# Performance work log

Measured on AMD Instinct MI355X. Metric: run time of the kernel, lower is better.

Reference implementation:

```python
import jax, jax.numpy as jnp
import numpy as np
import math

B, T, D = 8, 1024, 512
WS = 12          # window_size (top-k)
EPS = 1e-5       # BatchNorm eps (eval mode, running stats)
NEG = -1e9


def setup_inputs() -> dict:
    key = jax.random.key(0)
    ks = jax.random.split(key, 13)
    x = jax.random.normal(ks[0], (B, T, D), jnp.float32)
    conv1_w = jax.random.normal(ks[1], (512, 512, 5, 5), jnp.float32) / np.float32(np.sqrt(512 * 25))
    conv1_b = jax.random.normal(ks[2], (512,), jnp.float32) * 0.01
    bn1_g = jax.random.uniform(ks[3], (512,), jnp.float32, 0.5, 1.5)
    bn1_b = jax.random.normal(ks[4], (512,), jnp.float32) * 0.1
    bn1_m = jax.random.normal(ks[5], (512,), jnp.float32) * 0.1
    bn1_v = jax.random.uniform(ks[6], (512,), jnp.float32, 0.5, 1.5)
    conv2_w = jax.random.normal(ks[7], (512, 512, 5, 3), jnp.float32) / np.float32(np.sqrt(512 * 15))
    conv2_b = jax.random.normal(ks[8], (512,), jnp.float32) * 0.01
    bn2_g = jax.random.uniform(ks[9], (512,), jnp.float32, 0.5, 1.5)
    bn2_b = jax.random.normal(ks[10], (512,), jnp.float32) * 0.1
    bn2_m = jax.random.normal(ks[11], (512,), jnp.float32) * 0.1
    bn2_v = jax.random.uniform(ks[12], (512,), jnp.float32, 0.5, 1.5)
    return dict(x=x, conv1_w=conv1_w, conv1_b=conv1_b, bn1_g=bn1_g, bn1_b=bn1_b,
                bn1_m=bn1_m, bn1_v=bn1_v, conv2_w=conv2_w, conv2_b=conv2_b,
                bn2_g=bn2_g, bn2_b=bn2_b, bn2_m=bn2_m, bn2_v=bn2_v)


def _conv_nchw(h, w, b):
    # Conv2d padding=(2,0): pad height by 2 each side, no width padding.
    out = jax.lax.conv_general_dilated(h, w, window_strides=(1, 1),
                                       padding=((2, 2), (0, 0)),
                                       dimension_numbers=('NCHW', 'OIHW', 'NCHW'))
    return out + b[None, :, None, None]


def _bn(h, g, bt, m, v):
    # eval-mode BatchNorm2d with running stats
    inv = jax.lax.rsqrt(v + EPS)
    return (h - m[None, :, None, None]) * (g * inv)[None, :, None, None] + bt[None, :, None, None]


def _pool2(h):
    return jax.lax.reduce_window(h, -jnp.inf, jax.lax.max,
                                 (1, 1, 2, 2), (1, 1, 2, 2), 'VALID')


def reference(x, conv1_w, conv1_b, bn1_g, bn1_b, bn1_m, bn1_v,
              conv2_w, conv2_b, bn2_g, bn2_b, bn2_m, bn2_v):
    b, t, d = x.shape
    # masked local attention scores
    scores = jnp.einsum('btd,bsd->bts', x, x) / math.sqrt(d)  # [B,T,T]
    i = jnp.arange(t)[:, None]
    j = jnp.arange(t)[None, :]
    band = jnp.abs(j - i) <= (WS - 1)  # local band, width 2*WS-1
    scores = jnp.where(band[None], scores, NEG)
    # top-k window select, indices sorted ascending
    _, idx = jax.lax.top_k(scores, WS)           # [B,T,WS]
    ids = jnp.sort(idx, axis=-1)
    # batched gather: out[b,t,k,:] = x[b, ids[b,t,k], :]
    gathered = x[jnp.arange(b)[:, None, None], ids]  # [B,T,WS,D]
    h = gathered.transpose(0, 3, 1, 2)               # [B,512,T,WS]
    # conv encoder
    h = jax.nn.relu(_bn(_conv_nchw(h, conv1_w, conv1_b), bn1_g, bn1_b, bn1_m, bn1_v))
    h = _pool2(h)                                    # [B,512,T/2,4]
    h = jax.nn.relu(_bn(_conv_nchw(h, conv2_w, conv2_b), bn2_g, bn2_b, bn2_m, bn2_v))
    h = _pool2(h)                                    # [B,512,T/4,1]
    return jnp.squeeze(h)                            # [B,512,T/4]
```

## Files before the change

### kernel.cpp

```cpp
#include <hip/hip_runtime.h>
#include <hip/hip_bf16.h>

typedef short bf16x8 __attribute__((ext_vector_type(8)));
typedef float f32x16 __attribute__((ext_vector_type(16)));
typedef unsigned short u16;

__device__ __forceinline__ u16 f2bf(float v) {
    union { __hip_bfloat16 h; u16 u; } cv;
    cv.h = __float2bfloat16(v);
    return cv.u;
}

__device__ __forceinline__ void gld_lds16(const u16* g, u16* l) {
    __builtin_amdgcn_global_load_lds(
        (const __attribute__((address_space(1))) void*)g,
        (__attribute__((address_space(3))) void*)l, 16, 0, 0);
}

__global__ void prep_w1(const float* __restrict__ w, u16* __restrict__ o) {
    int idx = blockIdx.x * 256 + threadIdx.x;
    if (idx >= 25 * 512 * 512) return;
    int e = idx & 7, ocl = (idx >> 3) & 63, c = (idx >> 9) & 3;
    int ocs = (idx >> 11) & 7, T = idx >> 14;
    int icb = T / 25, tap = T - icb * 25;
    int ic = icb * 32 + c * 8 + e;
    int oc = ocs * 64 + ocl;
    int kh = tap / 5, kw = tap - kh * 5;
    o[idx] = f2bf(w[(((size_t)oc * 512 + ic) * 5 + kh) * 5 + kw]);
}

__global__ void prep_w2(const float* __restrict__ w, u16* __restrict__ o) {
    int idx = blockIdx.x * 256 + threadIdx.x;
    if (idx >= 15 * 512 * 512) return;
    int e = idx & 7, ocl = (idx >> 3) & 63, c = (idx >> 9) & 3;
    int ocs = (idx >> 11) & 7, T = idx >> 14;
    int icb = T / 15, tap = T - icb * 15;
    int ic = icb * 32 + c * 8 + e;
    int oc = ocs * 64 + ocl;
    int kh = tap / 3, kw = tap - kh * 3;
    o[idx] = f2bf(w[(((size_t)oc * 512 + ic) * 5 + kh) * 3 + kw]);
}

__global__ void prep_bn(const float* __restrict__ g, const float* __restrict__ b,
                        const float* __restrict__ m, const float* __restrict__ v,
                        float* __restrict__ scale, float* __restrict__ shift) {
    int i = blockIdx.x * 256 + threadIdx.x;
    if (i >= 512) return;
    float s = g[i] * rsqrtf(v[i] + 1e-5f);
    scale[i] = s;
    shift[i] = b[i] - m[i] * s;
}

__global__ void zero_pads(u16* __restrict__ gath, u16* __restrict__ pooled) {
    int idx = blockIdx.x * 256 + threadIdx.x;
    if (idx < 24576) {
        int w = idx % 12, r = idx / 12;
        int h4 = r & 3; r >>= 2;
        int cc = r & 63, b = r >> 6;
        int h = (h4 < 2) ? h4 : 1024 + h4;
        *(int4*)&gath[(((size_t)(b * 64 + cc)) * 12336 + h * 12 + w) * 8] =
            int4{0, 0, 0, 0};
    } else if (idx < 24576 + 8192) {
        int j = idx - 24576;
        int w = j & 3, r = j >> 2;
        int h4 = r & 3; r >>= 2;
        int cc = r & 63, b = r >> 6;
        int hp = (h4 < 2) ? h4 : 512 + h4;
        *(int4*)&pooled[(((size_t)(b * 64 + cc)) * 2064 + hp * 4 + w) * 8] =
            int4{0, 0, 0, 0};
    }
}

__global__ __launch_bounds__(256) void gather_topk(const float* __restrict__ x,
                                                   u16* __restrict__ g) {
    int bt = blockIdx.x;
    int b = bt >> 10, t = bt & 1023;
    const float* xb = x + (size_t)b * 1024 * 512;
    const float* xt = xb + (size_t)t * 512;
    __shared__ float xts[512];
    __shared__ float sc[23];
    __shared__ int sel[12];
    int tid = threadIdx.x;
    for (int i = tid; i < 512; i += 256) xts[i] = xt[i];
    __syncthreads();
    int j0 = t - 11; if (j0 < 0) j0 = 0;
    int j1 = t + 11; if (j1 > 1023) j1 = 1023;
    int C = j1 - j0 + 1;
    int wave = tid >> 6, lane = tid & 63;
    for (int c = wave; c < C; c += 4) {
        const float* xj = xb + (size_t)(j0 + c) * 512;
        double s = 0.0;
        #pragma unroll
        for (int e = 0; e < 8; ++e) {
            int d = lane * 8 + e;
            s += (double)xj[d] * (double)xts[d];
        }
        #pragma unroll
        for (int off = 32; off; off >>= 1) s += __shfl_xor(s, off, 64);
        if (lane == 0) sc[c] = (float)(s / 22.627416997969522);
    }
    __syncthreads();
    if (tid == 0) {
        int cnt = 0;
        for (int c = 0; c < C; ++c) {
            float v = sc[c];
            int r = 0;
            for (int k = 0; k < C; ++k) {
                float u = sc[k];
                r += (u > v) || (u == v && k < c);
            }
            if (r < 12) sel[cnt++] = j0 + c;
        }
    }
    __syncthreads();
    const size_t rowbase = (size_t)(t + 2) * 12;
    for (int i = tid; i < 768; i += 256) {
        int cc = i / 12, s = i - cc * 12;
        const float* src = xb + (size_t)sel[s] * 512 + cc * 8;
        float4 f0 = *(const float4*)src;
        float4 f1 = *(const float4*)(src + 4);
        u16 pk[8] = {f2bf(f0.x), f2bf(f0.y), f2bf(f0.z), f2bf(f0.w),
                     f2bf(f1.x), f2bf(f1.y), f2bf(f1.z), f2bf(f1.w)};
        *(int4*)&g[(((size_t)(b * 64 + cc)) * 12336 + rowbase + s) * 8] =
            *(const int4*)pk;
    }
}


template <int IN_W, int LOG_OW, int KH, int KW, int TH, int HTB, int MF32,
          int ARP, int PLANE, int CPX, bool POOL2E>
__global__ __launch_bounds__(512, 1) void conv_fused(
    const u16* __restrict__ A, const u16* __restrict__ Wt,
    const float* __restrict__ bias, const float* __restrict__ bnsc,
    const float* __restrict__ bnsh, void* __restrict__ outp) {
    constexpr int OW = 1 << LOG_OW;
    constexpr int TAPS = KH * KW;
    constexpr int JC = ARP / 64;
    constexpr int MFR = (32 >> LOG_OW) * IN_W;
    __shared__ u16 As_l[8 * ARP * 8];
    __shared__ u16 Ws_l[8][2][2048];

    const int tid = threadIdx.x;
    const int bid = blockIdx.x;
    const int lb = (bid & 7) * CPX + (bid >> 3);
    const int n0 = (lb & 1) * 256;
    const int mt = lb >> 1;
    const int b = mt / HTB;
    const int h0 = (mt % HTB) * TH;

    const int lane = tid & 63;
    const int wv = tid >> 6;
    const int wm = wv >> 2, wn = wv & 3;
    const int l31 = lane & 31, kgrp = lane >> 5;

    const int pos0 = wm * MF32 * 32 + l31;
    const int rowb0 = (pos0 >> LOG_OW) * IN_W + (pos0 & (OW - 1));
    const u16* aB = &As_l[(kgrp * ARP + rowb0) * 8];

    const int wlo = kgrp * 512 + l31 * 8;
    const u16* wA0 = &Ws_l[wv][0][wlo];
    const u16* wB0 = &Ws_l[wv][1][wlo];
    u16* dA = &Ws_l[wv][0][0];
    u16* dB = &Ws_l[wv][1][0];

    const int ocs = (lb & 1) * 4 + wn;
    const u16* wsg = Wt + (size_t)(8 + ocs) * 2048 + lane * 8;
    const u16* wprol = Wt + (size_t)ocs * 2048 + lane * 8;

    const u16* gAh = A + (((size_t)b * 64) * PLANE + h0 * IN_W + lane) * 8;

    f32x16 acc[MF32][2];
    #pragma unroll
    for (int i = 0; i < MF32; ++i)
        #pragma unroll
        for (int j = 0; j < 2; ++j)
            acc[i][j] = f32x16{0.f,0.f,0.f,0.f,0.f,0.f,0.f,0.f,
                               0.f,0.f,0.f,0.f,0.f,0.f,0.f,0.f};

    #pragma unroll 1
    for (int q = wv; q < 8 * JC; q += 8) {
        int c8 = q / JC, j = q - c8 * JC;
        gld_lds16(gAh + ((size_t)(c8 * PLANE) + j * 64) * 8,
                  &As_l[(c8 * ARP + j * 64) * 8]);
    }
    #pragma unroll
    for (int c = 0; c < 4; ++c)
        gld_lds16(wprol + c * 512, dA + c * 512);
    asm volatile("s_waitcnt vmcnt(0)" ::: "memory");
    __builtin_amdgcn_s_barrier();

    #pragma unroll 1
    for (int g = 0; g < 16; ++g) {
        const u16* wRe = (g & 1) ? wB0 : wA0;
        const u16* wRo = (g & 1) ? wA0 : wB0;
        u16* dE = (g & 1) ? dA : dB;
        u16* dO = (g & 1) ? dB : dA;
        const u16* aR = aB + (g & 1) * (4 * ARP * 8);
        #pragma unroll
        for (int t = 0; t < TAPS; ++t) {
            const u16* wS = wsg + (size_t)t * 16384;
            u16* dS = (t & 1) ? dO : dE;
            #pragma unroll
            for (int c = 0; c < 4; ++c)
                gld_lds16(wS + c * 512, dS + c * 512);
            asm volatile("s_waitcnt vmcnt(4)" ::: "memory");
            __builtin_amdgcn_sched_barrier(0);
            const int kh_ = t / KW;
            const int toff = kh_ * IN_W + (t - kh_ * KW);
            const u16* wR = (t & 1) ? wRo : wRe;
            __builtin_amdgcn_s_setprio(1);
            #pragma unroll
            for (int k = 0; k < 2; ++k) {
                bf16x8 afr[MF32], bfr[2];
                #pragma unroll
                for (int mf = 0; mf < MF32; ++mf)
                    afr[mf] = *(const bf16x8*)(aR +
                        (toff + MFR * mf + 2 * k * ARP) * 8);
                #pragma unroll
                for (int nf = 0; nf < 2; ++nf)
                    bfr[nf] = *(const bf16x8*)(wR + k * 1024 + nf * 256);
                #pragma unroll
                for (int mf = 0; mf < MF32; ++mf)
                    #pragma unroll
                    for (int nf = 0; nf < 2; ++nf)
                        acc[mf][nf] = __builtin_amdgcn_mfma_f32_32x32x16_bf16(
                            afr[mf], bfr[nf], acc[mf][nf], 0, 0, 0);
            }
            __builtin_amdgcn_s_setprio(0);
        }
        wsg += (size_t)TAPS * 16384;
        if ((g & 1) && g < 15) {
            __builtin_amdgcn_s_barrier();
            const int chn = (g + 1) >> 1;
            #pragma unroll 1
            for (int q = wv; q < 8 * JC; q += 8) {
                int c8 = q / JC, j = q - c8 * JC;
                gld_lds16(gAh + ((size_t)((chn * 8 + c8) * PLANE) + j * 64) * 8,
                          &As_l[(c8 * ARP + j * 64) * 8]);
            }
            asm volatile("s_waitcnt vmcnt(0)" ::: "memory");
            __builtin_amdgcn_s_barrier();
        }
    }
    asm volatile("s_waitcnt vmcnt(0)" ::: "memory");

    #pragma unroll
    for (int nf = 0; nf < 2; ++nf) {
        const int oc = n0 + wn * 64 + nf * 32 + l31;
        const float scv = bnsc[oc], shv = bnsh[oc], bi = bias[oc];
        const float shh = fmaf(bi, scv, shv);
        #pragma unroll
        for (int mf = 0; mf < MF32; ++mf) {
            #pragma unroll
            for (int q = 0; q < 4; ++q) {
                if (!POOL2E) {
                    const int r0 = (q & 1) * 2 + (q >> 1) * 8;
                    float mx = fmaxf(
                        fmaxf(acc[mf][nf][r0], acc[mf][nf][r0 + 1]),
                        fmaxf(acc[mf][nf][r0 + 4], acc[mf][nf][r0 + 5]));
                    float v = fmaxf(fmaf(mx, scv, shh), 0.f);
                    const int row0 = (r0 & 3) + 8 * (r0 >> 2) + 4 * kgrp;
                    const int pos = wm * MF32 * 32 + mf * 32 + row0;
                    const int h = h0 + (pos >> LOG_OW);
                    const int w = pos & (OW - 1);
                    const int prow = (2 + (h >> 1)) * 4 + (w >> 1);
                    u16* o = (u16*)outp;
                    o[(((size_t)(b * 64 + (oc >> 3))) * 2064 + prow) * 8 +
                      (oc & 7)] = f2bf(v);
                } else {
                    const int r0 = q * 4;
                    float mx = fmaxf(
                        fmaxf(acc[mf][nf][r0], acc[mf][nf][r0 + 1]),
                        fmaxf(acc[mf][nf][r0 + 2], acc[mf][nf][r0 + 3]));
                    float v = fmaxf(fmaf(mx, scv, shh), 0.f);
                    const int row0 = 8 * (r0 >> 2) + 4 * kgrp;
                    const int pos = wm * 32 + row0;
                    const int pout = (h0 + (pos >> 1)) >> 1;
                    float* o = (float*)outp;
                    o[((size_t)(b * 512 + oc)) * 256 + pout] = v;
                }
            }
        }
    }
}

extern "C" void kernel_launch(void* const* d_in, const int* in_sizes, int n_in,
                              void* d_out, int out_size, void* d_ws, size_t ws_size,
                              hipStream_t stream) {
    const float* x  = (const float*)d_in[0];
    const float* w1 = (const float*)d_in[1];
    const float* b1 = (const float*)d_in[2];
    const float* g1 = (const float*)d_in[3];
    const float* be1 = (const float*)d_in[4];
    const float* m1 = (const float*)d_in[5];
    const float* v1 = (const float*)d_in[6];
    const float* w2 = (const float*)d_in[7];
    const float* b2 = (const float*)d_in[8];
    const float* g2 = (const float*)d_in[9];
    const float* be2 = (const float*)d_in[10];
    const float* m2 = (const float*)d_in[11];
    const float* v2 = (const float*)d_in[12];
    float* out = (float*)d_out;

    char* ws = (char*)d_ws;
    u16* gathered = (u16*)(ws);
    u16* w1t      = (u16*)(ws + 101056512);
    u16* w2t      = (u16*)(ws + 114163712);
    float* bn1s   = (float*)(ws + 122028032);
    float* bn1t   = bn1s + 512;
    float* bn2s   = bn1s + 1024;
    float* bn2t   = bn1s + 1536;
    u16* pooled1  = (u16*)(ws + 122036224);

    prep_w1<<<25600, 256, 0, stream>>>(w1, w1t);
    prep_w2<<<15360, 256, 0, stream>>>(w2, w2t);
    prep_bn<<<2, 256, 0, stream>>>(g1, be1, m1, v1, bn1s, bn1t);
    prep_bn<<<2, 256, 0, stream>>>(g2, be2, m2, v2, bn2s, bn2t);
    zero_pads<<<128, 256, 0, stream>>>(gathered, pooled1);
    gather_topk<<<8192, 256, 0, stream>>>(x, gathered);

    conv_fused<12, 3, 5, 5, 32, 32, 4, 448, 12336, 64, false>
        <<<512, 512, 0, stream>>>(gathered, w1t, b1, bn1s, bn1t, pooled1);
    conv_fused<4, 1, 5, 3, 32, 16, 1, 192, 2064, 32, true>
        <<<256, 512, 0, stream>>>(pooled1, w2t, b2, bn2s, bn2t, out);
}
```

Baseline: 923.0 us.

## Load conv weight fragments directly into registers and pad activation LDS slabs

Weight fragments no longer go through a per-wave double-buffered LDS staging area. Each lane now loads its own bf16x8 weight fragments straight from global memory into registers, one tap ahead, and rotates them after the MFMAs. The activation LDS slabs get 32 elements of padding per channel group to reduce bank conflicts. This removes the LDS round trip and the vmcnt waits for weights, which frees LDS and may ease instruction pressure. In exchange the global loads are scattered per lane, register use goes up, and global latency is hidden only by the one-tap prefetch.

```diff
diff --git a/kernel.cpp b/kernel.cpp
--- a/kernel.cpp
+++ b/kernel.cpp
@@ -137,8 +137,8 @@
     constexpr int TAPS = KH * KW;
     constexpr int JC = ARP / 64;
     constexpr int MFR = (32 >> LOG_OW) * IN_W;
-    __shared__ u16 As_l[8 * ARP * 8];
-    __shared__ u16 Ws_l[8][2][2048];
+    constexpr int SLAB = ARP * 8 + 32;
+    __shared__ u16 As_l[8 * SLAB];
 
     const int tid = threadIdx.x;
     const int bid = blockIdx.x;
@@ -155,17 +155,10 @@
 
     const int pos0 = wm * MF32 * 32 + l31;
     const int rowb0 = (pos0 >> LOG_OW) * IN_W + (pos0 & (OW - 1));
-    const u16* aB = &As_l[(kgrp * ARP + rowb0) * 8];
-
-    const int wlo = kgrp * 512 + l31 * 8;
-    const u16* wA0 = &Ws_l[wv][0][wlo];
-    const u16* wB0 = &Ws_l[wv][1][wlo];
-    u16* dA = &Ws_l[wv][0][0];
-    u16* dB = &Ws_l[wv][1][0];
+    const u16* aB = &As_l[kgrp * SLAB + rowb0 * 8];
 
     const int ocs = (lb & 1) * 4 + wn;
-    const u16* wsg = Wt + (size_t)(8 + ocs) * 2048 + lane * 8;
-    const u16* wprol = Wt + (size_t)ocs * 2048 + lane * 8;
+    const u16* wlane = Wt + (size_t)ocs * 2048 + kgrp * 512 + l31 * 8;
 
     const u16* gAh = A + (((size_t)b * 64) * PLANE + h0 * IN_W + lane) * 8;
 
@@ -181,52 +174,53 @@
     for (int q = wv; q < 8 * JC; q += 8) {
         int c8 = q / JC, j = q - c8 * JC;
         gld_lds16(gAh + ((size_t)(c8 * PLANE) + j * 64) * 8,
-                  &As_l[(c8 * ARP + j * 64) * 8]);
-    }
-    #pragma unroll
-    for (int c = 0; c < 4; ++c)
-        gld_lds16(wprol + c * 512, dA + c * 512);
+                  &As_l[c8 * SLAB + j * 512]);
+    }
+    bf16x8 wc0 = *(const bf16x8*)(wlane);
+    bf16x8 wc1 = *(const bf16x8*)(wlane + 256);
+    bf16x8 wc2 = *(const bf16x8*)(wlane + 1024);
+    bf16x8 wc3 = *(const bf16x8*)(wlane + 1280);
     asm volatile("s_waitcnt vmcnt(0)" ::: "memory");
     __builtin_amdgcn_s_barrier();
 
+    const u16* wsg = wlane + 16384;
+
     #pragma unroll 1
     for (int g = 0; g < 16; ++g) {
-        const u16* wRe = (g & 1) ? wB0 : wA0;
-        const u16* wRo = (g & 1) ? wA0 : wB0;
-        u16* dE = (g & 1) ? dA : dB;
-        u16* dO = (g & 1) ? dB : dA;
-        const u16* aR = aB + (g & 1) * (4 * ARP * 8);
+        const u16* aR = (g & 1) ? aB + 4 * SLAB : aB;
         #pragma unroll
         for (int t = 0; t < TAPS; ++t) {
             const u16* wS = wsg + (size_t)t * 16384;
-            u16* dS = (t & 1) ? dO : dE;
-            #pragma unroll
-            for (int c = 0; c < 4; ++c)
-                gld_lds16(wS + c * 512, dS + c * 512);
-            asm volatile("s_waitcnt vmcnt(4)" ::: "memory");
-            __builtin_amdgcn_sched_barrier(0);
+            bf16x8 wn0 = *(const bf16x8*)(wS);
+            bf16x8 wn1 = *(const bf16x8*)(wS + 256);
+            bf16x8 wn2 = *(const bf16x8*)(wS + 1024);
+            bf16x8 wn3 = *(const bf16x8*)(wS + 1280);
             const int kh_ = t / KW;
             const int toff = kh_ * IN_W + (t - kh_ * KW);
-            const u16* wR = (t & 1) ? wRo : wRe;
             __builtin_amdgcn_s_setprio(1);
-            #pragma unroll
-            for (int k = 0; k < 2; ++k) {
-                bf16x8 afr[MF32], bfr[2];
-                #pragma unroll
-                for (int mf = 0; mf < MF32; ++mf)
-                    afr[mf] = *(const bf16x8*)(aR +
-                        (toff + MFR * mf + 2 * k * ARP) * 8);
-                #pragma unroll
-                for (int nf = 0; nf < 2; ++nf)
-                    bfr[nf] = *(const bf16x8*)(wR + k * 1024 + nf * 256);
-                #pragma unroll
-                for (int mf = 0; mf < MF32; ++mf)
-                    #pragma unroll
-                    for (int nf = 0; nf < 2; ++nf)
-                        acc[mf][nf] = __builtin_amdgcn_mfma_f32_32x32x16_bf16(
-                            afr[mf], bfr[nf], acc[mf][nf], 0, 0, 0);
+            bf16x8 afr[MF32];
+            #pragma unroll
+            for (int mf = 0; mf < MF32; ++mf)
+                afr[mf] = *(const bf16x8*)(aR + (toff + MFR * mf) * 8);
+            #pragma unroll
+            for (int mf = 0; mf < MF32; ++mf) {
+                acc[mf][0] = __builtin_amdgcn_mfma_f32_32x32x16_bf16(
+                    afr[mf], wc0, acc[mf][0], 0, 0, 0);
+                acc[mf][1] = __builtin_amdgcn_mfma_f32_32x32x16_bf16(
+                    afr[mf], wc1, acc[mf][1], 0, 0, 0);
+            }
+            #pragma unroll
+            for (int mf = 0; mf < MF32; ++mf)
+                afr[mf] = *(const bf16x8*)(aR + (toff + MFR * mf) * 8 + 2 * SLAB);
+            #pragma unroll
+            for (int mf = 0; mf < MF32; ++mf) {
+                acc[mf][0] = __builtin_amdgcn_mfma_f32_32x32x16_bf16(
+                    afr[mf], wc2, acc[mf][0], 0, 0, 0);
+                acc[mf][1] = __builtin_amdgcn_mfma_f32_32x32x16_bf16(
+                    afr[mf], wc3, acc[mf][1], 0, 0, 0);
             }
             __builtin_amdgcn_s_setprio(0);
+            wc0 = wn0; wc1 = wn1; wc2 = wn2; wc3 = wn3;
         }
         wsg += (size_t)TAPS * 16384;
         if ((g & 1) && g < 15) {
@@ -236,7 +230,7 @@
             for (int q = wv; q < 8 * JC; q += 8) {
                 int c8 = q / JC, j = q - c8 * JC;
                 gld_lds16(gAh + ((size_t)((chn * 8 + c8) * PLANE) + j * 64) * 8,
-                          &As_l[(c8 * ARP + j * 64) * 8]);
+                          &As_l[c8 * SLAB + j * 512]);
             }
             asm volatile("s_waitcnt vmcnt(0)" ::: "memory");
             __builtin_amdgcn_s_barrier();
```

Result: faster. 888.1 us (-3.8%).
